# Kernel tuning notes

Hardware: AMD Instinct MI355X
Metric: run time of the kernel (lower is better)

## Reference

```python
import jax, jax.numpy as jnp
from jax import lax
import numpy as np

SEQ, FEAT, VOCAB = 59, 64, 578
B, U = 4096, 1024


def setup_inputs() -> dict:
    key = jax.random.key(0)
    ks = jax.random.split(key, 6)
    x = jax.random.normal(ks[0], (B, SEQ, FEAT), dtype=jnp.float32)
    # Keras LSTMCell params: kernel [feat, 4U], recurrent_kernel [U, 4U], bias [4U]
    kernel = jax.random.normal(ks[1], (FEAT, 4 * U), dtype=jnp.float32) * 0.05
    rec_kernel = jax.random.normal(ks[2], (U, 4 * U), dtype=jnp.float32) * 0.05
    bias = jnp.zeros((4 * U,), dtype=jnp.float32)
    w2 = jax.random.normal(ks[3], (U, VOCAB), dtype=jnp.float32) * 0.05
    b2 = jnp.zeros((VOCAB,), dtype=jnp.float32)
    return {"x": x, "kernel": kernel, "rec_kernel": rec_kernel, "bias": bias, "w2": w2, "b2": b2}


def reference(x, kernel, rec_kernel, bias, w2, b2):
    batch = x.shape[0]
    units = rec_kernel.shape[0]
    xs = jnp.transpose(x, (1, 0, 2))  # [SEQ, B, FEAT]
    h0 = jnp.zeros((batch, units), dtype=x.dtype)
    c0 = jnp.zeros((batch, units), dtype=x.dtype)

    def step(carry, xt):
        h, c = carry
        z = xt @ kernel + h @ rec_kernel + bias  # [B, 4U]
        i, f, g, o = jnp.split(z, 4, axis=-1)    # Keras gate order i,f,c,o
        i = jax.nn.sigmoid(i)
        f = jax.nn.sigmoid(f)
        g = jnp.tanh(g)
        o = jax.nn.sigmoid(o)
        c_new = f * c + i * g
        h_new = o * jnp.tanh(c_new)
        return (h_new, c_new), None

    (h_last, _), _ = lax.scan(step, (h0, c0), xs)
    probs = jax.nn.softmax(h_last @ w2 + b2, axis=-1)  # dense2 softmax on last hidden
    # original: stack single prediction -> [1,B,V], transpose [1,0,2] -> [B,1,V]
    return probs[:, None, :]
```

## Files before the change

### kernel.cpp

```cpp
#include <hip/hip_runtime.h>

#define SEQ    59
#define FEAT   64
#define VOCAB  578
#define BATCH  4096
#define UNITS  1024
#define KLSTM  1088
#define NPAD   640

typedef __bf16 bf16x8 __attribute__((ext_vector_type(8)));
typedef __bf16 bf16x4 __attribute__((ext_vector_type(4)));
typedef float  floatx4 __attribute__((ext_vector_type(4)));

typedef const __attribute__((address_space(1))) char gas_char;
typedef __attribute__((address_space(3))) char las_char;

__device__ __forceinline__ float sigmoid_f(float x) { return 1.f / (1.f + __expf(-x)); }
__device__ __forceinline__ float tanh_f(float x) { float e = __expf(2.f * x); return 1.f - 2.f / (e + 1.f); }


__global__ void convert_x_kernel(const float* __restrict__ x, __bf16* __restrict__ xbf) {
    int i = blockIdx.x * 256 + threadIdx.x;
    const int total = BATCH * SEQ * FEAT / 4;
    if (i >= total) return;
    float4 v = ((const float4*)x)[i];
    bf16x4 o;
    o.x = (__bf16)v.x; o.y = (__bf16)v.y; o.z = (__bf16)v.z; o.w = (__bf16)v.w;
    ((bf16x4*)xbf)[i] = o;
}

__global__ void convert_weights_kernel(const float* __restrict__ kern,
                                       const float* __restrict__ reck,
                                       __bf16* __restrict__ Wtp) {
    int idx = blockIdx.x * 256 + threadIdx.x;
    if (idx >= 4096 * KLSTM) return;
    int np = idx / KLSTM;
    int k  = idx - np * KLSTM;
    int ublk = np >> 7;
    int g    = (np >> 5) & 3;
    int j    = np & 31;
    int n    = g * 1024 + ublk * 32 + j;
    float v = (k < FEAT) ? kern[(size_t)k * 4096 + n]
                         : reck[(size_t)(k - FEAT) * 4096 + n];
    Wtp[idx] = (__bf16)v;
}

__global__ void convert_w2_kernel(const float* __restrict__ w2, __bf16* __restrict__ Wt2p) {
    int idx = blockIdx.x * 256 + threadIdx.x;
    if (idx >= NPAD * 1024) return;
    int n = idx >> 10;
    int k = idx & 1023;
    float v = (n < VOCAB) ? w2[(size_t)k * VOCAB + n] : 0.f;
    Wt2p[idx] = (__bf16)v;
}

__global__ void __launch_bounds__(256, 2) lstm_step_kernel(
    const __bf16* __restrict__ xbf,
    const __bf16* __restrict__ Wtp,
    const float*  __restrict__ bias,
    const __bf16* __restrict__ hin,
    __bf16*       __restrict__ hout,
    float*        __restrict__ cstate,
    int t)
{
    __shared__ __bf16 As[128 * 64];
    __shared__ __bf16 Bs[2][128 * 64];

    const int tid  = threadIdx.x;
    const int wid  = tid >> 6;
    const int lane = tid & 63;
    const int ln   = lane & 15;
    const int lk   = lane >> 4;
    const int wm   = wid >> 1;
    const int wn   = wid & 1;
    const int rb   = blockIdx.x;
    const int yb   = blockIdx.y;

    floatx4 acc[2][4][4];
#pragma unroll
    for (int p = 0; p < 2; ++p)
#pragma unroll
        for (int m = 0; m < 4; ++m)
#pragma unroll
            for (int g = 0; g < 4; ++g)
                acc[p][m][g] = (floatx4){0.f, 0.f, 0.f, 0.f};

    int s_row[4], s_kgd[4];
#pragma unroll
    for (int q = 0; q < 4; ++q) {
        int flat = q * 256 + tid;
        int row  = flat >> 3;
        s_row[q] = row;
        s_kgd[q] = (flat & 7) ^ (row & 7);
    }

    for (int kt = 0; kt < 17; ++kt) {
        __syncthreads();
#pragma unroll
        for (int q = 0; q < 4; ++q) {
            const int row = s_row[q], kgd = s_kgd[q];
            const __bf16* gp;
            if (kt == 0)
                gp = xbf + (size_t)(rb * 128 + row) * (SEQ * FEAT) + t * FEAT + kgd * 8;
            else
                gp = hin + ((size_t)(rb * 128 + row) << 10) + (kt - 1) * 64 + kgd * 8;
            __builtin_amdgcn_global_load_lds((gas_char*)gp,
                (las_char*)(As + (size_t)(q * 256 + (wid << 6)) * 8), 16, 0, 0);
        }
#pragma unroll
        for (int p = 0; p < 2; ++p) {
#pragma unroll
            for (int q = 0; q < 4; ++q) {
                const int n = s_row[q], kgd = s_kgd[q];
                const __bf16* gp = Wtp + (size_t)(yb * 256 + p * 128 + n) * KLSTM + kt * 64 + kgd * 8;
                __builtin_amdgcn_global_load_lds((gas_char*)gp,
                    (las_char*)(Bs[p] + (size_t)(q * 256 + (wid << 6)) * 8), 16, 0, 0);
            }
        }
        __syncthreads();
#pragma unroll
        for (int kk = 0; kk < 2; ++kk) {
            const int kg = kk * 4 + lk;
            bf16x8 a[4], b0[4], b1[4];
#pragma unroll
            for (int m = 0; m < 4; ++m) {
                int row  = wm * 64 + m * 16 + ln;
                int ccol = (kg ^ (row & 7)) * 8;
                a[m] = *(const bf16x8*)(As + row * 64 + ccol);
            }
#pragma unroll
            for (int g = 0; g < 4; ++g) {
                int n    = g * 32 + wn * 16 + ln;
                int ccol = (kg ^ (n & 7)) * 8;
                b0[g] = *(const bf16x8*)(Bs[0] + n * 64 + ccol);
                b1[g] = *(const bf16x8*)(Bs[1] + n * 64 + ccol);
            }
#pragma unroll
            for (int m = 0; m < 4; ++m)
#pragma unroll
                for (int g = 0; g < 4; ++g) {
                    acc[0][m][g] = __builtin_amdgcn_mfma_f32_16x16x32_bf16(a[m], b0[g], acc[0][m][g], 0, 0, 0);
                    acc[1][m][g] = __builtin_amdgcn_mfma_f32_16x16x32_bf16(a[m], b1[g], acc[1][m][g], 0, 0, 0);
                }
        }
    }

#pragma unroll
    for (int p = 0; p < 2; ++p) {
        const int u  = (yb * 2 + p) * 32 + wn * 16 + ln;
        const float bi  = bias[u];
        const float bfv = bias[UNITS + u];
        const float bg  = bias[2 * UNITS + u];
        const float bo  = bias[3 * UNITS + u];
#pragma unroll
        for (int m = 0; m < 4; ++m) {
            const int row0 = rb * 128 + wm * 64 + m * 16 + lk * 4;
#pragma unroll
            for (int r = 0; r < 4; ++r) {
                const size_t idx = ((size_t)(row0 + r) << 10) + u;
                float ig = sigmoid_f(acc[p][m][0][r] + bi);
                float fg = sigmoid_f(acc[p][m][1][r] + bfv);
                float gg = tanh_f(acc[p][m][2][r] + bg);
                float og = sigmoid_f(acc[p][m][3][r] + bo);
                float cn = fg * cstate[idx] + ig * gg;
                cstate[idx] = cn;
                hout[idx] = (__bf16)(og * tanh_f(cn));
            }
        }
    }
}

__global__ void __launch_bounds__(256) dense_kernel(
    const __bf16* __restrict__ hin,
    const __bf16* __restrict__ Wt2p,
    float*        __restrict__ logits)
{
    __shared__ __bf16 As[128 * 64];
    __shared__ __bf16 Bs[128 * 64];

    const int tid  = threadIdx.x;
    const int wid  = tid >> 6;
    const int lane = tid & 63;
    const int ln   = lane & 15;
    const int lk   = lane >> 4;
    const int wm   = wid >> 1;
    const int wn   = wid & 1;
    const int rb   = blockIdx.x;
    const int nb   = blockIdx.y;

    floatx4 acc[4][4];
#pragma unroll
    for (int m = 0; m < 4; ++m)
#pragma unroll
        for (int g = 0; g < 4; ++g)
            acc[m][g] = (floatx4){0.f, 0.f, 0.f, 0.f};

    int s_row[4], s_kgd[4];
#pragma unroll
    for (int q = 0; q < 4; ++q) {
        int flat = q * 256 + tid;
        int row  = flat >> 3;
        s_row[q] = row;
        s_kgd[q] = (flat & 7) ^ (row & 7);
    }

    for (int kt = 0; kt < 16; ++kt) {
        __syncthreads();
#pragma unroll
        for (int q = 0; q < 4; ++q) {
            const int row = s_row[q], kgd = s_kgd[q];
            const __bf16* gp = hin + ((size_t)(rb * 128 + row) << 10) + kt * 64 + kgd * 8;
            __builtin_amdgcn_global_load_lds((gas_char*)gp,
                (las_char*)(As + (size_t)(q * 256 + (wid << 6)) * 8), 16, 0, 0);
        }
#pragma unroll
        for (int q = 0; q < 4; ++q) {
            const int n = s_row[q], kgd = s_kgd[q];
            const __bf16* gp = Wt2p + ((size_t)(nb * 128 + n) << 10) + kt * 64 + kgd * 8;
            __builtin_amdgcn_global_load_lds((gas_char*)gp,
                (las_char*)(Bs + (size_t)(q * 256 + (wid << 6)) * 8), 16, 0, 0);
        }
        __syncthreads();
#pragma unroll
        for (int kk = 0; kk < 2; ++kk) {
            const int kg = kk * 4 + lk;
            bf16x8 a[4], b[4];
#pragma unroll
            for (int m = 0; m < 4; ++m) {
                int row  = wm * 64 + m * 16 + ln;
                int ccol = (kg ^ (row & 7)) * 8;
                a[m] = *(const bf16x8*)(As + row * 64 + ccol);
            }
#pragma unroll
            for (int g = 0; g < 4; ++g) {
                int n    = g * 32 + wn * 16 + ln;
                int ccol = (kg ^ (n & 7)) * 8;
                b[g] = *(const bf16x8*)(Bs + n * 64 + ccol);
            }
#pragma unroll
            for (int m = 0; m < 4; ++m)
#pragma unroll
                for (int g = 0; g < 4; ++g)
                    acc[m][g] = __builtin_amdgcn_mfma_f32_16x16x32_bf16(a[m], b[g], acc[m][g], 0, 0, 0);
        }
    }

#pragma unroll
    for (int m = 0; m < 4; ++m) {
        const int row0 = rb * 128 + wm * 64 + m * 16 + lk * 4;
#pragma unroll
        for (int g = 0; g < 4; ++g) {
            const int n = nb * 128 + g * 32 + wn * 16 + ln;
#pragma unroll
            for (int r = 0; r < 4; ++r)
                logits[(size_t)(row0 + r) * NPAD + n] = acc[m][g][r];
        }
    }
}

__global__ void __launch_bounds__(256) softmax_kernel(
    const float* __restrict__ logits,
    const float* __restrict__ b2,
    float* __restrict__ out)
{
    const int row = blockIdx.x;
    const int tid = threadIdx.x;
    __shared__ float red[8];

    float z[3];
    float lmax = -1e30f;
#pragma unroll
    for (int j = 0; j < 3; ++j) {
        int col = tid + j * 256;
        if (col < VOCAB) {
            z[j] = logits[(size_t)row * NPAD + col] + b2[col];
            lmax = fmaxf(lmax, z[j]);
        } else z[j] = -1e30f;
    }
    for (int off = 32; off > 0; off >>= 1) lmax = fmaxf(lmax, __shfl_xor(lmax, off));
    if ((tid & 63) == 0) red[tid >> 6] = lmax;
    __syncthreads();
    lmax = fmaxf(fmaxf(red[0], red[1]), fmaxf(red[2], red[3]));
    __syncthreads();

    float lsum = 0.f;
#pragma unroll
    for (int j = 0; j < 3; ++j) {
        int col = tid + j * 256;
        if (col < VOCAB) { z[j] = __expf(z[j] - lmax); lsum += z[j]; }
    }
    for (int off = 32; off > 0; off >>= 1) lsum += __shfl_xor(lsum, off);
    if ((tid & 63) == 0) red[tid >> 6] = lsum;
    __syncthreads();
    lsum = red[0] + red[1] + red[2] + red[3];
    float inv = 1.f / lsum;
#pragma unroll
    for (int j = 0; j < 3; ++j) {
        int col = tid + j * 256;
        if (col < VOCAB) out[(size_t)row * VOCAB + col] = z[j] * inv;
    }
}

extern "C" void kernel_launch(void* const* d_in, const int* in_sizes, int n_in,
                              void* d_out, int out_size, void* d_ws, size_t ws_size,
                              hipStream_t stream)
{
    const float* x    = (const float*)d_in[0];
    const float* kern = (const float*)d_in[1];
    const float* reck = (const float*)d_in[2];
    const float* bias = (const float*)d_in[3];
    const float* w2   = (const float*)d_in[4];
    const float* b2   = (const float*)d_in[5];
    float* out = (float*)d_out;

    char* ws = (char*)d_ws;
    size_t off = 0;
    auto alloc = [&](size_t bytes) {
        char* p = ws + off;
        off += (bytes + 255) & ~(size_t)255;
        return p;
    };
    __bf16* Wtp    = (__bf16*)alloc((size_t)4096 * KLSTM * 2);
    __bf16* Wt2p   = (__bf16*)alloc((size_t)NPAD * 1024 * 2);
    __bf16* xbf    = (__bf16*)alloc((size_t)BATCH * SEQ * FEAT * 2);
    __bf16* h0     = (__bf16*)alloc((size_t)BATCH * UNITS * 2);
    __bf16* h1     = (__bf16*)alloc((size_t)BATCH * UNITS * 2);
    float*  cst    = (float*)alloc((size_t)BATCH * UNITS * 4);
    float*  logits = (float*)alloc((size_t)BATCH * NPAD * 4);
    if (off > ws_size) return;

    (void)hipMemsetAsync(h0, 0, (size_t)BATCH * UNITS * 2, stream);
    (void)hipMemsetAsync(cst, 0, (size_t)BATCH * UNITS * 4, stream);

    convert_x_kernel<<<(BATCH * SEQ * FEAT / 4 + 255) / 256, 256, 0, stream>>>(x, xbf);
    convert_weights_kernel<<<(4096 * KLSTM + 255) / 256, 256, 0, stream>>>(kern, reck, Wtp);
    convert_w2_kernel<<<(NPAD * 1024 + 255) / 256, 256, 0, stream>>>(w2, Wt2p);

    __bf16* hin = h0; __bf16* hout = h1;
    for (int t = 0; t < SEQ; ++t) {
        lstm_step_kernel<<<dim3(32, 16), 256, 0, stream>>>(xbf, Wtp, bias, hin, hout, cst, t);
        __bf16* tmp = hin; hin = hout; hout = tmp;
    }

    dense_kernel<<<dim3(32, 5), 256, 0, stream>>>(hin, Wt2p, logits);
    softmax_kernel<<<BATCH, 256, 0, stream>>>(logits, b2, out);
}
```

Before: 2.664 ms.

## Rewrite LSTM step GEMM as 256x256 tile with double-buffered, barrier-phased pipeline

The per-timestep LSTM GEMM now uses 512-thread blocks, each computing a 256-row by 256-gate-column tile. The 64-wide K slices are split into halves and double-buffered in LDS, with global-to-LDS prefetches interleaved between MFMA phases, explicit vmcnt/lgkmcnt waits and setprio hints. The weight layout is re-permuted and K is padded to 1152, and the hidden buffers get a padded row stride, to match the new tiling. The aim is to hide load latency and raise data reuse per block. The cost is many more barriers per iteration and fewer blocks in the grid (256 instead of 512), which gives fewer waves to cover latency.

```diff
diff --git a/kernel.cpp b/kernel.cpp
--- a/kernel.cpp
+++ b/kernel.cpp
@@ -6,6 +6,8 @@
 #define BATCH  4096
 #define UNITS  1024
 #define KLSTM  1088
+#define KPAD   1152
+#define HSTRIDE 1088
 #define NPAD   640
 
 typedef __bf16 bf16x8 __attribute__((ext_vector_type(8)));
@@ -17,6 +19,12 @@
 
 __device__ __forceinline__ float sigmoid_f(float x) { return 1.f / (1.f + __expf(-x)); }
 __device__ __forceinline__ float tanh_f(float x) { float e = __expf(2.f * x); return 1.f - 2.f / (e + 1.f); }
+
+#define GLDS(srcp, dstp) __builtin_amdgcn_global_load_lds((gas_char*)(srcp), (las_char*)(dstp), 16, 0, 0)
+#define BAR()  __builtin_amdgcn_s_barrier()
+#define LGKM0() asm volatile("s_waitcnt lgkmcnt(0)" ::: "memory")
+#define VM6()  asm volatile("s_waitcnt vmcnt(6)" ::: "memory")
+#define MFMA   __builtin_amdgcn_mfma_f32_16x16x32_bf16
 
 
 __global__ void convert_x_kernel(const float* __restrict__ x, __bf16* __restrict__ xbf) {
@@ -33,15 +41,17 @@
                                        const float* __restrict__ reck,
                                        __bf16* __restrict__ Wtp) {
     int idx = blockIdx.x * 256 + threadIdx.x;
-    if (idx >= 4096 * KLSTM) return;
-    int np = idx / KLSTM;
-    int k  = idx - np * KLSTM;
-    int ublk = np >> 7;
-    int g    = (np >> 5) & 3;
-    int j    = np & 31;
-    int n    = g * 1024 + ublk * 32 + j;
-    float v = (k < FEAT) ? kern[(size_t)k * 4096 + n]
-                         : reck[(size_t)(k - FEAT) * 4096 + n];
+    if (idx >= 4096 * KPAD) return;
+    int np = idx / KPAD;
+    int k  = idx - np * KPAD;
+    int bc = np >> 8;
+    int w  = (np >> 6) & 3;
+    int g  = (np >> 4) & 3;
+    int j  = np & 15;
+    int n  = g * 1024 + bc * 64 + w * 16 + j;
+    float v = 0.f;
+    if (k < FEAT)       v = kern[(size_t)k * 4096 + n];
+    else if (k < KLSTM) v = reck[(size_t)(k - FEAT) * 4096 + n];
     Wtp[idx] = (__bf16)v;
 }
 
@@ -54,7 +64,7 @@
     Wt2p[idx] = (__bf16)v;
 }
 
-__global__ void __launch_bounds__(256, 2) lstm_step_kernel(
+__global__ void __launch_bounds__(512, 2) lstm_step_kernel(
     const __bf16* __restrict__ xbf,
     const __bf16* __restrict__ Wtp,
     const float*  __restrict__ bias,
@@ -63,111 +73,188 @@
     float*        __restrict__ cstate,
     int t)
 {
-    __shared__ __bf16 As[128 * 64];
-    __shared__ __bf16 Bs[2][128 * 64];
+    __shared__ __bf16 Ash[2][2][256 * 32];
+    __shared__ __bf16 Bsh[2][2][128 * 64];
 
     const int tid  = threadIdx.x;
     const int wid  = tid >> 6;
     const int lane = tid & 63;
     const int ln   = lane & 15;
     const int lk   = lane >> 4;
-    const int wm   = wid >> 1;
-    const int wn   = wid & 1;
+    const int wm   = wid >> 2;
+    const int wn   = wid & 3;
     const int rb   = blockIdx.x;
-    const int yb   = blockIdx.y;
-
-    floatx4 acc[2][4][4];
-#pragma unroll
-    for (int p = 0; p < 2; ++p)
-#pragma unroll
-        for (int m = 0; m < 4; ++m)
-#pragma unroll
-            for (int g = 0; g < 4; ++g)
-                acc[p][m][g] = (floatx4){0.f, 0.f, 0.f, 0.f};
-
-    int s_row[4], s_kgd[4];
-#pragma unroll
-    for (int q = 0; q < 4; ++q) {
-        int flat = q * 256 + tid;
-        int row  = flat >> 3;
-        s_row[q] = row;
-        s_kgd[q] = (flat & 7) ^ (row & 7);
-    }
-
-    for (int kt = 0; kt < 17; ++kt) {
-        __syncthreads();
-#pragma unroll
-        for (int q = 0; q < 4; ++q) {
-            const int row = s_row[q], kgd = s_kgd[q];
-            const __bf16* gp;
-            if (kt == 0)
-                gp = xbf + (size_t)(rb * 128 + row) * (SEQ * FEAT) + t * FEAT + kgd * 8;
-            else
-                gp = hin + ((size_t)(rb * 128 + row) << 10) + (kt - 1) * 64 + kgd * 8;
-            __builtin_amdgcn_global_load_lds((gas_char*)gp,
-                (las_char*)(As + (size_t)(q * 256 + (wid << 6)) * 8), 16, 0, 0);
-        }
-#pragma unroll
-        for (int p = 0; p < 2; ++p) {
-#pragma unroll
-            for (int q = 0; q < 4; ++q) {
-                const int n = s_row[q], kgd = s_kgd[q];
-                const __bf16* gp = Wtp + (size_t)(yb * 256 + p * 128 + n) * KLSTM + kt * 64 + kgd * 8;
-                __builtin_amdgcn_global_load_lds((gas_char*)gp,
-                    (las_char*)(Bs[p] + (size_t)(q * 256 + (wid << 6)) * 8), 16, 0, 0);
-            }
-        }
-        __syncthreads();
-#pragma unroll
-        for (int kk = 0; kk < 2; ++kk) {
-            const int kg = kk * 4 + lk;
-            bf16x8 a[4], b0[4], b1[4];
-#pragma unroll
-            for (int m = 0; m < 4; ++m) {
-                int row  = wm * 64 + m * 16 + ln;
-                int ccol = (kg ^ (row & 7)) * 8;
-                a[m] = *(const bf16x8*)(As + row * 64 + ccol);
-            }
-#pragma unroll
-            for (int g = 0; g < 4; ++g) {
-                int n    = g * 32 + wn * 16 + ln;
-                int ccol = (kg ^ (n & 7)) * 8;
-                b0[g] = *(const bf16x8*)(Bs[0] + n * 64 + ccol);
-                b1[g] = *(const bf16x8*)(Bs[1] + n * 64 + ccol);
-            }
-#pragma unroll
-            for (int m = 0; m < 4; ++m)
-#pragma unroll
-                for (int g = 0; g < 4; ++g) {
-                    acc[0][m][g] = __builtin_amdgcn_mfma_f32_16x16x32_bf16(a[m], b0[g], acc[0][m][g], 0, 0, 0);
-                    acc[1][m][g] = __builtin_amdgcn_mfma_f32_16x16x32_bf16(a[m], b1[g], acc[1][m][g], 0, 0, 0);
-                }
-        }
-    }
-
-#pragma unroll
-    for (int p = 0; p < 2; ++p) {
-        const int u  = (yb * 2 + p) * 32 + wn * 16 + ln;
-        const float bi  = bias[u];
-        const float bfv = bias[UNITS + u];
-        const float bg  = bias[2 * UNITS + u];
-        const float bo  = bias[3 * UNITS + u];
-#pragma unroll
-        for (int m = 0; m < 4; ++m) {
-            const int row0 = rb * 128 + wm * 64 + m * 16 + lk * 4;
-#pragma unroll
-            for (int r = 0; r < 4; ++r) {
-                const size_t idx = ((size_t)(row0 + r) << 10) + u;
-                float ig = sigmoid_f(acc[p][m][0][r] + bi);
-                float fg = sigmoid_f(acc[p][m][1][r] + bfv);
-                float gg = tanh_f(acc[p][m][2][r] + bg);
-                float og = sigmoid_f(acc[p][m][3][r] + bo);
-                float cn = fg * cstate[idx] + ig * gg;
-                cstate[idx] = cn;
-                hout[idx] = (__bf16)(og * tanh_f(cn));
-            }
-        }
-    }
+    const int bc   = blockIdx.y;
+
+    floatx4 acc[8][4];
+#pragma unroll
+    for (int m = 0; m < 8; ++m)
+#pragma unroll
+        for (int g = 0; g < 4; ++g)
+            acc[m][g] = (floatx4){0.f, 0.f, 0.f, 0.f};
+
+    const int af0 = tid, af1 = 512 + tid;
+    const int ar0 = af0 >> 2, ar1 = af1 >> 2;
+    const int ac0 = (af0 & 3) ^ ((ar0 >> 1) & 3);
+    const int ac1 = (af1 & 3) ^ ((ar1 >> 1) & 3);
+    const int br0 = af0 >> 3, br1 = af1 >> 3;
+    const int bc0 = (af0 & 7) ^ (br0 & 7);
+    const int bc1 = (af1 & 7) ^ (br1 & 7);
+
+    const __bf16* hA0 = hin + (size_t)(rb * 256 + ar0) * HSTRIDE + ac0 * 8;
+    const __bf16* hA1 = hin + (size_t)(rb * 256 + ar1) * HSTRIDE + ac1 * 8;
+    const __bf16* xA0 = xbf + (size_t)(rb * 256 + ar0) * (SEQ * FEAT) + t * FEAT + ac0 * 8;
+    const __bf16* xA1 = xbf + (size_t)(rb * 256 + ar1) * (SEQ * FEAT) + t * FEAT + ac1 * 8;
+    const __bf16* wB0 = Wtp + (size_t)(bc * 256 + br0) * KPAD + bc0 * 8;
+    const __bf16* wB1 = Wtp + (size_t)(bc * 256 + br1) * KPAD + bc1 * 8;
+
+    const int adst0 = (wid << 9);
+    const int adst1 = 4096 + (wid << 9);
+
+#define STA(BUF, KH, COLB) do { \
+    GLDS(hA0 + (COLB) + (KH) * 32, &Ash[BUF][KH][adst0]); \
+    GLDS(hA1 + (COLB) + (KH) * 32, &Ash[BUF][KH][adst1]); } while (0)
+#define STB(BUF, NH, COLB) do { \
+    GLDS(wB0 + (size_t)(NH) * 128 * KPAD + (COLB), &Bsh[BUF][NH][adst0]); \
+    GLDS(wB1 + (size_t)(NH) * 128 * KPAD + (COLB), &Bsh[BUF][NH][adst1]); } while (0)
+
+    int offA[8];
+#pragma unroll
+    for (int m = 0; m < 8; ++m) {
+        int row = wm * 128 + m * 16 + ln;
+        offA[m] = row * 32 + ((lk ^ ((row >> 1) & 3)) << 3);
+    }
+    int offB[4][2];
+#pragma unroll
+    for (int g = 0; g < 4; ++g) {
+        int nr = (wn & 1) * 64 + g * 16 + ln;
+#pragma unroll
+        for (int kk = 0; kk < 2; ++kk)
+            offB[g][kk] = nr * 64 + ((((kk << 2) + lk) ^ (nr & 7)) << 3);
+    }
+    const int nhsel = wn >> 1;
+    const __bf16* B0  = Bsh[0][nhsel];
+    const __bf16* B1  = Bsh[1][nhsel];
+    const __bf16* A00 = Ash[0][0];
+    const __bf16* A01 = Ash[0][1];
+    const __bf16* A10 = Ash[1][0];
+    const __bf16* A11 = Ash[1][1];
+
+    STB(0, 1, 0);
+    GLDS(xA0, &Ash[0][0][adst0]); GLDS(xA1, &Ash[0][0][adst1]);
+    STB(0, 0, 0);
+    GLDS(xA0 + 32, &Ash[0][1][adst0]); GLDS(xA1 + 32, &Ash[0][1][adst1]);
+    STB(1, 1, 64);
+    STA(1, 0, 0);
+    STB(1, 0, 64);
+    VM6();
+    BAR();
+
+#define PHASE_MFMA(MB, KKB) \
+    __builtin_amdgcn_s_setprio(1); \
+    _Pragma("unroll") \
+    for (int m = 0; m < 4; ++m) \
+    _Pragma("unroll") \
+        for (int g = 0; g < 4; ++g) \
+            acc[(MB) + m][g] = MFMA(aa[m], bb[KKB][g], acc[(MB) + m][g], 0, 0, 0); \
+    __builtin_amdgcn_s_setprio(0)
+
+#pragma unroll 1
+    for (int it = 0; it < 9; ++it) {
+        const int t2 = (2 * it + 2 <= 17) ? (2 * it + 2) : 17;
+        const int t3 = (2 * it + 3 <= 17) ? (2 * it + 3) : 17;
+        const int cA1 = it * 128;
+        const int cB2 = t2 * 64, cA2 = (t2 - 1) * 64;
+        const int cB3 = t3 * 64, cA3 = (t3 - 1) * 64;
+        bf16x8 bb[2][4], aa[4];
+
+#pragma unroll
+        for (int g = 0; g < 4; ++g) {
+            bb[0][g] = *(const bf16x8*)(B0 + offB[g][0]);
+            bb[1][g] = *(const bf16x8*)(B0 + offB[g][1]);
+        }
+#pragma unroll
+        for (int m = 0; m < 4; ++m) aa[m] = *(const bf16x8*)(A00 + offA[m]);
+        STA(1, 1, cA1);
+        BAR(); LGKM0();
+        PHASE_MFMA(0, 0);
+        BAR();
+#pragma unroll
+        for (int m = 0; m < 4; ++m) aa[m] = *(const bf16x8*)(A00 + offA[4 + m]);
+        STB(0, 1, cB2);
+        BAR(); LGKM0();
+        PHASE_MFMA(4, 0);
+        BAR();
+#pragma unroll
+        for (int m = 0; m < 4; ++m) aa[m] = *(const bf16x8*)(A01 + offA[m]);
+        STA(0, 0, cA2);
+        BAR(); LGKM0();
+        PHASE_MFMA(0, 1);
+        BAR();
+#pragma unroll
+        for (int m = 0; m < 4; ++m) aa[m] = *(const bf16x8*)(A01 + offA[4 + m]);
+        STB(0, 0, cB2);
+        BAR(); LGKM0();
+        PHASE_MFMA(4, 1);
+        VM6();
+        BAR();
+
+#pragma unroll
+        for (int g = 0; g < 4; ++g) {
+            bb[0][g] = *(const bf16x8*)(B1 + offB[g][0]);
+            bb[1][g] = *(const bf16x8*)(B1 + offB[g][1]);
+        }
+#pragma unroll
+        for (int m = 0; m < 4; ++m) aa[m] = *(const bf16x8*)(A10 + offA[m]);
+        STA(0, 1, cA2);
+        BAR(); LGKM0();
+        PHASE_MFMA(0, 0);
+        BAR();
+#pragma unroll
+        for (int m = 0; m < 4; ++m) aa[m] = *(const bf16x8*)(A10 + offA[4 + m]);
+        STB(1, 1, cB3);
+        BAR(); LGKM0();
+        PHASE_MFMA(4, 0);
+        BAR();
+#pragma unroll
+        for (int m = 0; m < 4; ++m) aa[m] = *(const bf16x8*)(A11 + offA[m]);
+        STA(1, 0, cA3);
+        BAR(); LGKM0();
+        PHASE_MFMA(0, 1);
+        BAR();
+#pragma unroll
+        for (int m = 0; m < 4; ++m) aa[m] = *(const bf16x8*)(A11 + offA[4 + m]);
+        STB(1, 0, cB3);
+        BAR(); LGKM0();
+        PHASE_MFMA(4, 1);
+        VM6();
+        BAR();
+    }
+
+    asm volatile("s_waitcnt vmcnt(0)" ::: "memory");
+
+    const int u = bc * 64 + wn * 16 + ln;
+    const float bi  = bias[u];
+    const float bfv = bias[UNITS + u];
+    const float bg  = bias[2 * UNITS + u];
+    const float bo  = bias[3 * UNITS + u];
+#pragma unroll
+    for (int m = 0; m < 8; ++m) {
+        const int row0 = rb * 256 + wm * 128 + m * 16 + lk * 4;
+#pragma unroll
+        for (int r = 0; r < 4; ++r) {
+            const size_t ic = (size_t)(row0 + r) * UNITS + u;
+            float ig = sigmoid_f(acc[m][0][r] + bi);
+            float fg = sigmoid_f(acc[m][1][r] + bfv);
+            float gg = tanh_f(acc[m][2][r] + bg);
+            float og = sigmoid_f(acc[m][3][r] + bo);
+            float cn = fg * cstate[ic] + ig * gg;
+            cstate[ic] = cn;
+            hout[(size_t)(row0 + r) * HSTRIDE + u] = (__bf16)(og * tanh_f(cn));
+        }
+    }
+#undef STA
+#undef STB
 }
 
 __global__ void __launch_bounds__(256) dense_kernel(
@@ -209,16 +296,14 @@
 #pragma unroll
         for (int q = 0; q < 4; ++q) {
             const int row = s_row[q], kgd = s_kgd[q];
-            const __bf16* gp = hin + ((size_t)(rb * 128 + row) << 10) + kt * 64 + kgd * 8;
-            __builtin_amdgcn_global_load_lds((gas_char*)gp,
-                (las_char*)(As + (size_t)(q * 256 + (wid << 6)) * 8), 16, 0, 0);
+            const __bf16* gp = hin + (size_t)(rb * 128 + row) * HSTRIDE + kt * 64 + kgd * 8;
+            GLDS(gp, As + (size_t)(q * 256 + (wid << 6)) * 8);
         }
 #pragma unroll
         for (int q = 0; q < 4; ++q) {
             const int n = s_row[q], kgd = s_kgd[q];
             const __bf16* gp = Wt2p + ((size_t)(nb * 128 + n) << 10) + kt * 64 + kgd * 8;
-            __builtin_amdgcn_global_load_lds((gas_char*)gp,
-                (las_char*)(Bs + (size_t)(q * 256 + (wid << 6)) * 8), 16, 0, 0);
+            GLDS(gp, Bs + (size_t)(q * 256 + (wid << 6)) * 8);
         }
         __syncthreads();
 #pragma unroll
@@ -241,7 +326,7 @@
             for (int m = 0; m < 4; ++m)
 #pragma unroll
                 for (int g = 0; g < 4; ++g)
-                    acc[m][g] = __builtin_amdgcn_mfma_f32_16x16x32_bf16(a[m], b[g], acc[m][g], 0, 0, 0);
+                    acc[m][g] = MFMA(a[m], b[g], acc[m][g], 0, 0, 0);
         }
     }
 
@@ -320,25 +405,26 @@
         off += (bytes + 255) & ~(size_t)255;
         return p;
     };
-    __bf16* Wtp    = (__bf16*)alloc((size_t)4096 * KLSTM * 2);
+    __bf16* Wtp    = (__bf16*)alloc((size_t)4096 * KPAD * 2);
     __bf16* Wt2p   = (__bf16*)alloc((size_t)NPAD * 1024 * 2);
     __bf16* xbf    = (__bf16*)alloc((size_t)BATCH * SEQ * FEAT * 2);
-    __bf16* h0     = (__bf16*)alloc((size_t)BATCH * UNITS * 2);
-    __bf16* h1     = (__bf16*)alloc((size_t)BATCH * UNITS * 2);
+    __bf16* h0     = (__bf16*)alloc((size_t)BATCH * HSTRIDE * 2);
+    __bf16* h1     = (__bf16*)alloc((size_t)BATCH * HSTRIDE * 2);
     float*  cst    = (float*)alloc((size_t)BATCH * UNITS * 4);
     float*  logits = (float*)alloc((size_t)BATCH * NPAD * 4);
     if (off > ws_size) return;
 
-    (void)hipMemsetAsync(h0, 0, (size_t)BATCH * UNITS * 2, stream);
+    (void)hipMemsetAsync(h0, 0, (size_t)BATCH * HSTRIDE * 2, stream);
+    (void)hipMemsetAsync(h1, 0, (size_t)BATCH * HSTRIDE * 2, stream);
     (void)hipMemsetAsync(cst, 0, (size_t)BATCH * UNITS * 4, stream);
 
     convert_x_kernel<<<(BATCH * SEQ * FEAT / 4 + 255) / 256, 256, 0, stream>>>(x, xbf);
-    convert_weights_kernel<<<(4096 * KLSTM + 255) / 256, 256, 0, stream>>>(kern, reck, Wtp);
+    convert_weights_kernel<<<(4096 * KPAD + 255) / 256, 256, 0, stream>>>(kern, reck, Wtp);
     convert_w2_kernel<<<(NPAD * 1024 + 255) / 256, 256, 0, stream>>>(w2, Wt2p);
 
     __bf16* hin = h0; __bf16* hout = h1;
     for (int t = 0; t < SEQ; ++t) {
-        lstm_step_kernel<<<dim3(32, 16), 256, 0, stream>>>(xbf, Wtp, bias, hin, hout, cst, t);
+        lstm_step_kernel<<<dim3(16, 16), 512, 0, stream>>>(xbf, Wtp, bias, hin, hout, cst, t);
         __bf16* tmp = hin; hin = hout; hout = tmp;
     }
 
```

Result: slower. 2.832 ms (+6.3%).

## Fuse LSTM timesteps into one persistent cooperative kernel with per-row-group barriers

Applied to the files above, without the earlier changes.

Replaces the 59 per-timestep kernel launches with a single persistent cooperative kernel. Blocks that share a batch row group synchronize through an atomic counter barrier, and the cell state stays in registers instead of being reloaded from global memory each step. The h output is staged through LDS so it can be written with coalesced cache-bypassing stores. This removes launch overhead and the global c-state traffic, at the cost of spin-wait synchronization and a dependence on every block being co-resident; the spin has a timeout escape and there is a non-cooperative fallback launch.

```diff
diff --git a/kernel.cpp b/kernel.cpp
--- a/kernel.cpp
+++ b/kernel.cpp
@@ -17,6 +17,11 @@
 
 __device__ __forceinline__ float sigmoid_f(float x) { return 1.f / (1.f + __expf(-x)); }
 __device__ __forceinline__ float tanh_f(float x) { float e = __expf(2.f * x); return 1.f - 2.f / (e + 1.f); }
+
+#define GLDS(srcp, dstp)  __builtin_amdgcn_global_load_lds((gas_char*)(srcp), (las_char*)(dstp), 16, 0, 0)
+#define GLDSC(srcp, dstp) __builtin_amdgcn_global_load_lds((gas_char*)(srcp), (las_char*)(dstp), 16, 0, 0x11)
+#define VMW(n)  asm volatile("s_waitcnt vmcnt(" #n ")" ::: "memory")
+#define MFMA    __builtin_amdgcn_mfma_f32_16x16x32_bf16
 
 
 __global__ void convert_x_kernel(const float* __restrict__ x, __bf16* __restrict__ xbf) {
@@ -54,14 +59,13 @@
     Wt2p[idx] = (__bf16)v;
 }
 
-__global__ void __launch_bounds__(256, 2) lstm_step_kernel(
+__global__ void __launch_bounds__(256, 2) lstm_seq_kernel(
     const __bf16* __restrict__ xbf,
     const __bf16* __restrict__ Wtp,
     const float*  __restrict__ bias,
-    const __bf16* __restrict__ hin,
-    __bf16*       __restrict__ hout,
-    float*        __restrict__ cstate,
-    int t)
+    __bf16*       __restrict__ hb0,
+    __bf16*       __restrict__ hb1,
+    unsigned*                  barGrp)
 {
     __shared__ __bf16 As[128 * 64];
     __shared__ __bf16 Bs[2][128 * 64];
@@ -73,17 +77,8 @@
     const int lk   = lane >> 4;
     const int wm   = wid >> 1;
     const int wn   = wid & 1;
-    const int rb   = blockIdx.x;
-    const int yb   = blockIdx.y;
-
-    floatx4 acc[2][4][4];
-#pragma unroll
-    for (int p = 0; p < 2; ++p)
-#pragma unroll
-        for (int m = 0; m < 4; ++m)
-#pragma unroll
-            for (int g = 0; g < 4; ++g)
-                acc[p][m][g] = (floatx4){0.f, 0.f, 0.f, 0.f};
+    const int yb   = blockIdx.x;
+    const int rb   = blockIdx.y;
 
     int s_row[4], s_kgd[4];
 #pragma unroll
@@ -94,30 +89,29 @@
         s_kgd[q] = (flat & 7) ^ (row & 7);
     }
 
-    for (int kt = 0; kt < 17; ++kt) {
-        __syncthreads();
-#pragma unroll
-        for (int q = 0; q < 4; ++q) {
-            const int row = s_row[q], kgd = s_kgd[q];
-            const __bf16* gp;
-            if (kt == 0)
-                gp = xbf + (size_t)(rb * 128 + row) * (SEQ * FEAT) + t * FEAT + kgd * 8;
-            else
-                gp = hin + ((size_t)(rb * 128 + row) << 10) + (kt - 1) * 64 + kgd * 8;
-            __builtin_amdgcn_global_load_lds((gas_char*)gp,
-                (las_char*)(As + (size_t)(q * 256 + (wid << 6)) * 8), 16, 0, 0);
-        }
-#pragma unroll
-        for (int p = 0; p < 2; ++p) {
-#pragma unroll
-            for (int q = 0; q < 4; ++q) {
-                const int n = s_row[q], kgd = s_kgd[q];
-                const __bf16* gp = Wtp + (size_t)(yb * 256 + p * 128 + n) * KLSTM + kt * 64 + kgd * 8;
-                __builtin_amdgcn_global_load_lds((gas_char*)gp,
-                    (las_char*)(Bs[p] + (size_t)(q * 256 + (wid << 6)) * 8), 16, 0, 0);
-            }
-        }
-        __syncthreads();
+    unsigned* grpCnt = barGrp + rb * 32;
+
+    float BI[2], BF_[2], BG[2], BO[2];
+#pragma unroll
+    for (int p = 0; p < 2; ++p) {
+        const int u = yb * 64 + p * 32 + wn * 16 + ln;
+        BI[p]  = bias[u];
+        BF_[p] = bias[UNITS + u];
+        BG[p]  = bias[2 * UNITS + u];
+        BO[p]  = bias[3 * UNITS + u];
+    }
+
+    float cc[2][4][4];
+#pragma unroll
+    for (int p = 0; p < 2; ++p)
+#pragma unroll
+        for (int m = 0; m < 4; ++m)
+#pragma unroll
+            for (int r = 0; r < 4; ++r) cc[p][m][r] = 0.f;
+
+    floatx4 acc[2][4][4];
+
+    auto compute_tile = [&]() {
 #pragma unroll
         for (int kk = 0; kk < 2; ++kk) {
             const int kg = kk * 4 + lk;
@@ -139,35 +133,105 @@
             for (int m = 0; m < 4; ++m)
 #pragma unroll
                 for (int g = 0; g < 4; ++g) {
-                    acc[0][m][g] = __builtin_amdgcn_mfma_f32_16x16x32_bf16(a[m], b0[g], acc[0][m][g], 0, 0, 0);
-                    acc[1][m][g] = __builtin_amdgcn_mfma_f32_16x16x32_bf16(a[m], b1[g], acc[1][m][g], 0, 0, 0);
+                    acc[0][m][g] = MFMA(a[m], b0[g], acc[0][m][g], 0, 0, 0);
+                    acc[1][m][g] = MFMA(a[m], b1[g], acc[1][m][g], 0, 0, 0);
                 }
         }
-    }
-
-#pragma unroll
-    for (int p = 0; p < 2; ++p) {
-        const int u  = (yb * 2 + p) * 32 + wn * 16 + ln;
-        const float bi  = bias[u];
-        const float bfv = bias[UNITS + u];
-        const float bg  = bias[2 * UNITS + u];
-        const float bo  = bias[3 * UNITS + u];
-#pragma unroll
-        for (int m = 0; m < 4; ++m) {
-            const int row0 = rb * 128 + wm * 64 + m * 16 + lk * 4;
-#pragma unroll
-            for (int r = 0; r < 4; ++r) {
-                const size_t idx = ((size_t)(row0 + r) << 10) + u;
-                float ig = sigmoid_f(acc[p][m][0][r] + bi);
-                float fg = sigmoid_f(acc[p][m][1][r] + bfv);
-                float gg = tanh_f(acc[p][m][2][r] + bg);
-                float og = sigmoid_f(acc[p][m][3][r] + bo);
-                float cn = fg * cstate[idx] + ig * gg;
-                cstate[idx] = cn;
-                hout[idx] = (__bf16)(og * tanh_f(cn));
-            }
-        }
-    }
+    };
+
+#define STAGE_B(KT) do { \
+    _Pragma("unroll") \
+    for (int p = 0; p < 2; ++p) \
+    _Pragma("unroll") \
+    for (int q = 0; q < 4; ++q) { \
+        const __bf16* gp = Wtp + (size_t)(yb * 256 + p * 128 + s_row[q]) * KLSTM + (KT) * 64 + s_kgd[q] * 8; \
+        GLDS(gp, Bs[p] + (size_t)(q * 256 + (wid << 6)) * 8); \
+    } } while (0)
+
+#pragma unroll 1
+    for (int t = 0; t < SEQ; ++t) {
+        const __bf16* hin  = (t & 1) ? hb1 : hb0;
+        __bf16*       hout = (t & 1) ? hb0 : hb1;
+
+#pragma unroll
+        for (int p = 0; p < 2; ++p)
+#pragma unroll
+            for (int m = 0; m < 4; ++m)
+#pragma unroll
+                for (int g = 0; g < 4; ++g)
+                    acc[p][m][g] = (floatx4){0.f, 0.f, 0.f, 0.f};
+
+#pragma unroll
+        for (int q = 0; q < 4; ++q) {
+            const __bf16* gp = xbf + (size_t)(rb * 128 + s_row[q]) * (SEQ * FEAT) + t * FEAT + s_kgd[q] * 8;
+            GLDS(gp, As + (size_t)(q * 256 + (wid << 6)) * 8);
+        }
+        STAGE_B(0);
+
+        if (tid == 0) {
+            const unsigned tgt = (unsigned)t * 16u;
+            unsigned spin = 0;
+            while (__hip_atomic_load(grpCnt, __ATOMIC_RELAXED, __HIP_MEMORY_SCOPE_AGENT) < tgt) {
+                __builtin_amdgcn_s_sleep(2);
+                if (++spin > (1u << 22)) break;
+            }
+        }
+        __syncthreads();
+
+        compute_tile();
+
+        for (int kt = 1; kt < 17; ++kt) {
+            __syncthreads();
+#pragma unroll
+            for (int q = 0; q < 4; ++q) {
+                const __bf16* gp = hin + ((size_t)(rb * 128 + s_row[q]) << 10) + (kt - 1) * 64 + s_kgd[q] * 8;
+                GLDSC(gp, As + (size_t)(q * 256 + (wid << 6)) * 8);
+            }
+            STAGE_B(kt);
+            __syncthreads();
+            compute_tile();
+        }
+
+        __syncthreads();
+        {
+            __bf16* h_lds = As;
+#pragma unroll
+            for (int p = 0; p < 2; ++p) {
+                const int cl = (p * 32 + wn * 16 + ln) ^ (lk << 4);
+#pragma unroll
+                for (int m = 0; m < 4; ++m) {
+                    const int r0 = wm * 64 + m * 16 + lk * 4;
+#pragma unroll
+                    for (int r = 0; r < 4; ++r) {
+                        float ig = sigmoid_f(acc[p][m][0][r] + BI[p]);
+                        float fg = sigmoid_f(acc[p][m][1][r] + BF_[p]);
+                        float gg = tanh_f(acc[p][m][2][r] + BG[p]);
+                        float og = sigmoid_f(acc[p][m][3][r] + BO[p]);
+                        float cn = fg * cc[p][m][r] + ig * gg;
+                        cc[p][m][r] = cn;
+                        h_lds[(r0 + r) * 64 + cl] = (__bf16)(og * tanh_f(cn));
+                    }
+                }
+            }
+            __syncthreads();
+#pragma unroll
+            for (int j = 0; j < 4; ++j) {
+                const int chunk = j * 256 + tid;
+                const int lrow  = chunk >> 3;
+                const int cof   = (chunk & 7) * 8;
+                const int pcol  = cof ^ (((lrow >> 2) & 3) << 4);
+                floatx4 v = *(const floatx4*)(h_lds + lrow * 64 + pcol);
+                const __bf16* hp = hout + (size_t)(rb * 128 + lrow) * UNITS + yb * 64 + cof;
+                asm volatile("global_store_dwordx4 %0, %1, off sc0 sc1"
+                             :: "v"(hp), "v"(v) : "memory");
+            }
+            VMW(0);
+            __syncthreads();
+            if (tid == 0)
+                __hip_atomic_fetch_add(grpCnt, 1u, __ATOMIC_RELAXED, __HIP_MEMORY_SCOPE_AGENT);
+        }
+    }
+#undef STAGE_B
 }
 
 __global__ void __launch_bounds__(256) dense_kernel(
@@ -210,15 +274,13 @@
         for (int q = 0; q < 4; ++q) {
             const int row = s_row[q], kgd = s_kgd[q];
             const __bf16* gp = hin + ((size_t)(rb * 128 + row) << 10) + kt * 64 + kgd * 8;
-            __builtin_amdgcn_global_load_lds((gas_char*)gp,
-                (las_char*)(As + (size_t)(q * 256 + (wid << 6)) * 8), 16, 0, 0);
+            GLDS(gp, As + (size_t)(q * 256 + (wid << 6)) * 8);
         }
 #pragma unroll
         for (int q = 0; q < 4; ++q) {
             const int n = s_row[q], kgd = s_kgd[q];
             const __bf16* gp = Wt2p + ((size_t)(nb * 128 + n) << 10) + kt * 64 + kgd * 8;
-            __builtin_amdgcn_global_load_lds((gas_char*)gp,
-                (las_char*)(Bs + (size_t)(q * 256 + (wid << 6)) * 8), 16, 0, 0);
+            GLDS(gp, Bs + (size_t)(q * 256 + (wid << 6)) * 8);
         }
         __syncthreads();
 #pragma unroll
@@ -241,7 +303,7 @@
             for (int m = 0; m < 4; ++m)
 #pragma unroll
                 for (int g = 0; g < 4; ++g)
-                    acc[m][g] = __builtin_amdgcn_mfma_f32_16x16x32_bf16(a[m], b[g], acc[m][g], 0, 0, 0);
+                    acc[m][g] = MFMA(a[m], b[g], acc[m][g], 0, 0, 0);
         }
     }
 
@@ -320,28 +382,34 @@
         off += (bytes + 255) & ~(size_t)255;
         return p;
     };
-    __bf16* Wtp    = (__bf16*)alloc((size_t)4096 * KLSTM * 2);
-    __bf16* Wt2p   = (__bf16*)alloc((size_t)NPAD * 1024 * 2);
-    __bf16* xbf    = (__bf16*)alloc((size_t)BATCH * SEQ * FEAT * 2);
-    __bf16* h0     = (__bf16*)alloc((size_t)BATCH * UNITS * 2);
-    __bf16* h1     = (__bf16*)alloc((size_t)BATCH * UNITS * 2);
-    float*  cst    = (float*)alloc((size_t)BATCH * UNITS * 4);
-    float*  logits = (float*)alloc((size_t)BATCH * NPAD * 4);
+    __bf16*   Wtp    = (__bf16*)alloc((size_t)4096 * KLSTM * 2);
+    __bf16*   Wt2p   = (__bf16*)alloc((size_t)NPAD * 1024 * 2);
+    __bf16*   xbf    = (__bf16*)alloc((size_t)BATCH * SEQ * FEAT * 2);
+    __bf16*   h0     = (__bf16*)alloc((size_t)BATCH * UNITS * 2);
+    __bf16*   h1     = (__bf16*)alloc((size_t)BATCH * UNITS * 2);
+    float*    logits = (float*)alloc((size_t)BATCH * NPAD * 4);
+    unsigned* barGrp = (unsigned*)alloc(32 * 128);
     if (off > ws_size) return;
 
     (void)hipMemsetAsync(h0, 0, (size_t)BATCH * UNITS * 2, stream);
-    (void)hipMemsetAsync(cst, 0, (size_t)BATCH * UNITS * 4, stream);
+    (void)hipMemsetAsync(barGrp, 0, 32 * 128, stream);
 
     convert_x_kernel<<<(BATCH * SEQ * FEAT / 4 + 255) / 256, 256, 0, stream>>>(x, xbf);
     convert_weights_kernel<<<(4096 * KLSTM + 255) / 256, 256, 0, stream>>>(kern, reck, Wtp);
     convert_w2_kernel<<<(NPAD * 1024 + 255) / 256, 256, 0, stream>>>(w2, Wt2p);
 
-    __bf16* hin = h0; __bf16* hout = h1;
-    for (int t = 0; t < SEQ; ++t) {
-        lstm_step_kernel<<<dim3(32, 16), 256, 0, stream>>>(xbf, Wtp, bias, hin, hout, cst, t);
-        __bf16* tmp = hin; hin = hout; hout = tmp;
-    }
-
-    dense_kernel<<<dim3(32, 5), 256, 0, stream>>>(hin, Wt2p, logits);
+    {
+        const __bf16* a0 = xbf; const __bf16* a1 = Wtp; const float* a2 = bias;
+        __bf16* a3 = h0; __bf16* a4 = h1; unsigned* a5 = barGrp;
+        void* args[6] = { (void*)&a0, (void*)&a1, (void*)&a2,
+                          (void*)&a3, (void*)&a4, (void*)&a5 };
+        hipError_t ce = hipLaunchCooperativeKernel((const void*)lstm_seq_kernel,
+                                                   dim3(16, 32), dim3(256),
+                                                   args, 0, stream);
+        if (ce != hipSuccess)
+            lstm_seq_kernel<<<dim3(16, 32), 256, 0, stream>>>(xbf, Wtp, bias, h0, h1, barGrp);
+    }
+
+    dense_kernel<<<dim3(32, 5), 256, 0, stream>>>(h1, Wt2p, logits);
     softmax_kernel<<<BATCH, 256, 0, stream>>>(logits, b2, out);
 }
```

Result: slower. 3.048 ms (+14.4%).

## Coalesce LSTM epilogue via LDS staging, tile-private cell state layout, swap grid order

Applied to the files above, without the earlier changes.

The LSTM step epilogue now stages h values through shared memory with an XOR swizzle and writes them to global memory as contiguous 16-byte chunks, replacing scattered 2-byte stores. The cell state is stored in a tile-private permuted layout, so each thread reads and writes contiguous float4 vectors. The grid dimensions are swapped so that consecutive blocks share the same batch rows and read different weight column tiles, which changes L2 reuse. The cost is an extra barrier and LDS round trip per step, and a cell state layout that only this kernel can read.

```diff
diff --git a/kernel.cpp b/kernel.cpp
--- a/kernel.cpp
+++ b/kernel.cpp
@@ -17,6 +17,9 @@
 
 __device__ __forceinline__ float sigmoid_f(float x) { return 1.f / (1.f + __expf(-x)); }
 __device__ __forceinline__ float tanh_f(float x) { float e = __expf(2.f * x); return 1.f - 2.f / (e + 1.f); }
+
+#define GLDS(srcp, dstp) __builtin_amdgcn_global_load_lds((gas_char*)(srcp), (las_char*)(dstp), 16, 0, 0)
+#define MFMA __builtin_amdgcn_mfma_f32_16x16x32_bf16
 
 
 __global__ void convert_x_kernel(const float* __restrict__ x, __bf16* __restrict__ xbf) {
@@ -73,8 +76,8 @@
     const int lk   = lane >> 4;
     const int wm   = wid >> 1;
     const int wn   = wid & 1;
-    const int rb   = blockIdx.x;
-    const int yb   = blockIdx.y;
+    const int yb   = blockIdx.x;
+    const int rb   = blockIdx.y;
 
     floatx4 acc[2][4][4];
 #pragma unroll
@@ -104,8 +107,7 @@
                 gp = xbf + (size_t)(rb * 128 + row) * (SEQ * FEAT) + t * FEAT + kgd * 8;
             else
                 gp = hin + ((size_t)(rb * 128 + row) << 10) + (kt - 1) * 64 + kgd * 8;
-            __builtin_amdgcn_global_load_lds((gas_char*)gp,
-                (las_char*)(As + (size_t)(q * 256 + (wid << 6)) * 8), 16, 0, 0);
+            GLDS(gp, As + (size_t)(q * 256 + (wid << 6)) * 8);
         }
 #pragma unroll
         for (int p = 0; p < 2; ++p) {
@@ -113,8 +115,7 @@
             for (int q = 0; q < 4; ++q) {
                 const int n = s_row[q], kgd = s_kgd[q];
                 const __bf16* gp = Wtp + (size_t)(yb * 256 + p * 128 + n) * KLSTM + kt * 64 + kgd * 8;
-                __builtin_amdgcn_global_load_lds((gas_char*)gp,
-                    (las_char*)(Bs[p] + (size_t)(q * 256 + (wid << 6)) * 8), 16, 0, 0);
+                GLDS(gp, Bs[p] + (size_t)(q * 256 + (wid << 6)) * 8);
             }
         }
         __syncthreads();
@@ -139,33 +140,51 @@
             for (int m = 0; m < 4; ++m)
 #pragma unroll
                 for (int g = 0; g < 4; ++g) {
-                    acc[0][m][g] = __builtin_amdgcn_mfma_f32_16x16x32_bf16(a[m], b0[g], acc[0][m][g], 0, 0, 0);
-                    acc[1][m][g] = __builtin_amdgcn_mfma_f32_16x16x32_bf16(a[m], b1[g], acc[1][m][g], 0, 0, 0);
+                    acc[0][m][g] = MFMA(a[m], b0[g], acc[0][m][g], 0, 0, 0);
+                    acc[1][m][g] = MFMA(a[m], b1[g], acc[1][m][g], 0, 0, 0);
                 }
         }
     }
 
-#pragma unroll
-    for (int p = 0; p < 2; ++p) {
-        const int u  = (yb * 2 + p) * 32 + wn * 16 + ln;
-        const float bi  = bias[u];
-        const float bfv = bias[UNITS + u];
-        const float bg  = bias[2 * UNITS + u];
-        const float bo  = bias[3 * UNITS + u];
-#pragma unroll
-        for (int m = 0; m < 4; ++m) {
-            const int row0 = rb * 128 + wm * 64 + m * 16 + lk * 4;
-#pragma unroll
-            for (int r = 0; r < 4; ++r) {
-                const size_t idx = ((size_t)(row0 + r) << 10) + u;
-                float ig = sigmoid_f(acc[p][m][0][r] + bi);
-                float fg = sigmoid_f(acc[p][m][1][r] + bfv);
-                float gg = tanh_f(acc[p][m][2][r] + bg);
-                float og = sigmoid_f(acc[p][m][3][r] + bo);
-                float cn = fg * cstate[idx] + ig * gg;
-                cstate[idx] = cn;
-                hout[idx] = (__bf16)(og * tanh_f(cn));
-            }
+    __syncthreads();
+    {
+        floatx4* cp = (floatx4*)cstate + ((size_t)(rb * 16 + yb) * 256 + tid) * 8;
+        __bf16* h_lds = As;
+#pragma unroll
+        for (int p = 0; p < 2; ++p) {
+            const int u  = (yb * 2 + p) * 32 + wn * 16 + ln;
+            const float bi  = bias[u];
+            const float bfv = bias[UNITS + u];
+            const float bg  = bias[2 * UNITS + u];
+            const float bo  = bias[3 * UNITS + u];
+            const int cl = (p * 32 + wn * 16 + ln) ^ (lk << 4);
+#pragma unroll
+            for (int m = 0; m < 4; ++m) {
+                const int r0 = wm * 64 + m * 16 + lk * 4;
+                floatx4 cold = cp[p * 4 + m];
+                floatx4 cnew;
+#pragma unroll
+                for (int r = 0; r < 4; ++r) {
+                    float ig = sigmoid_f(acc[p][m][0][r] + bi);
+                    float fg = sigmoid_f(acc[p][m][1][r] + bfv);
+                    float gg = tanh_f(acc[p][m][2][r] + bg);
+                    float og = sigmoid_f(acc[p][m][3][r] + bo);
+                    float cn = fg * cold[r] + ig * gg;
+                    cnew[r] = cn;
+                    h_lds[(r0 + r) * 64 + cl] = (__bf16)(og * tanh_f(cn));
+                }
+                cp[p * 4 + m] = cnew;
+            }
+        }
+        __syncthreads();
+#pragma unroll
+        for (int j = 0; j < 4; ++j) {
+            const int chunk = j * 256 + tid;
+            const int lrow  = chunk >> 3;
+            const int cof   = (chunk & 7) * 8;
+            const int pcol  = cof ^ (((lrow >> 2) & 3) << 4);
+            floatx4 v = *(const floatx4*)(h_lds + lrow * 64 + pcol);
+            *(floatx4*)(hout + (size_t)(rb * 128 + lrow) * UNITS + yb * 64 + cof) = v;
         }
     }
 }
@@ -210,15 +229,13 @@
         for (int q = 0; q < 4; ++q) {
             const int row = s_row[q], kgd = s_kgd[q];
             const __bf16* gp = hin + ((size_t)(rb * 128 + row) << 10) + kt * 64 + kgd * 8;
-            __builtin_amdgcn_global_load_lds((gas_char*)gp,
-                (las_char*)(As + (size_t)(q * 256 + (wid << 6)) * 8), 16, 0, 0);
+            GLDS(gp, As + (size_t)(q * 256 + (wid << 6)) * 8);
         }
 #pragma unroll
         for (int q = 0; q < 4; ++q) {
             const int n = s_row[q], kgd = s_kgd[q];
             const __bf16* gp = Wt2p + ((size_t)(nb * 128 + n) << 10) + kt * 64 + kgd * 8;
-            __builtin_amdgcn_global_load_lds((gas_char*)gp,
-                (las_char*)(Bs + (size_t)(q * 256 + (wid << 6)) * 8), 16, 0, 0);
+            GLDS(gp, Bs + (size_t)(q * 256 + (wid << 6)) * 8);
         }
         __syncthreads();
 #pragma unroll
@@ -241,7 +258,7 @@
             for (int m = 0; m < 4; ++m)
 #pragma unroll
                 for (int g = 0; g < 4; ++g)
-                    acc[m][g] = __builtin_amdgcn_mfma_f32_16x16x32_bf16(a[m], b[g], acc[m][g], 0, 0, 0);
+                    acc[m][g] = MFMA(a[m], b[g], acc[m][g], 0, 0, 0);
         }
     }
 
@@ -338,7 +355,7 @@
 
     __bf16* hin = h0; __bf16* hout = h1;
     for (int t = 0; t < SEQ; ++t) {
-        lstm_step_kernel<<<dim3(32, 16), 256, 0, stream>>>(xbf, Wtp, bias, hin, hout, cst, t);
+        lstm_step_kernel<<<dim3(16, 32), 256, 0, stream>>>(xbf, Wtp, bias, hin, hout, cst, t);
         __bf16* tmp = hin; hin = hout; hout = tmp;
     }
 
```

Result: slower. 2.741 ms (+2.9%).
